# Kernel optimization log

Measured on AMD Instinct MI355X. Metric: run time of the kernel, lower is better.

The kernel has to match this reference:

```python
import jax, jax.numpy as jnp
import numpy as np

INPUT_DIM = 100
LATENT_DIM = 128
HIDDEN_DIM = 64
BATCH = 16384


def setup_inputs() -> dict:
    key = jax.random.key(0)
    ku, k1, kb1, k2, kb2 = jax.random.split(key, 5)
    u = jax.random.normal(ku, (BATCH, INPUT_DIM), dtype=jnp.float32)
    # PyTorch Linear init: U(-1/sqrt(fan_in), 1/sqrt(fan_in))
    s1 = 1.0 / np.sqrt(INPUT_DIM)
    s2 = 1.0 / np.sqrt(HIDDEN_DIM)
    W1 = jax.random.uniform(k1, (LATENT_DIM, HIDDEN_DIM, INPUT_DIM), jnp.float32, -s1, s1)
    b1 = jax.random.uniform(kb1, (LATENT_DIM, HIDDEN_DIM), jnp.float32, -s1, s1)
    W2 = jax.random.uniform(k2, (LATENT_DIM, HIDDEN_DIM), jnp.float32, -s2, s2)  # out_features=1 squeezed
    b2 = jax.random.uniform(kb2, (LATENT_DIM,), jnp.float32, -s2, s2)
    return {"u": u, "W1": W1, "b1": b1, "W2": W2, "b2": b2}


def reference(u, W1, b1, W2, b2):
    # All latent_dim branches batched as one grouped GEMM.
    # h: [batch, latent, hidden]
    h = jnp.tanh(jnp.einsum('bi,khi->bkh', u, W1) + b1[None, :, :])
    # out: [batch, latent]  (second Linear has output dim 1, squeezed)
    out = jnp.einsum('bkh,kh->bk', h, W2) + b2[None, :]
    return out
```

## Files before the change

### kernel.cpp

```cpp
#include <hip/hip_runtime.h>

#define BATCH 16384
#define LATENT 128
#define HIDDEN 64
#define INDIM 100
#define KPAD 128

typedef short shortx8 __attribute__((ext_vector_type(8)));
typedef float floatx4 __attribute__((ext_vector_type(4)));

__device__ __forceinline__ short f2bf(float f) {
    union { float f; unsigned u; } v; v.f = f;
    unsigned r = v.u + 0x7FFF + ((v.u >> 16) & 1);
    return (short)(r >> 16);
}

#if __has_builtin(__builtin_amdgcn_exp2f)
#define EXP2F(x) __builtin_amdgcn_exp2f(x)
#else
#define EXP2F(x) __exp2f(x)
#endif
#if __has_builtin(__builtin_amdgcn_rcpf)
#define RCPF(x) __builtin_amdgcn_rcpf(x)
#else
#define RCPF(x) (1.0f / (x))
#endif

#define DPP_REDUCE16(v) do {                                                              \
    v += __int_as_float(__builtin_amdgcn_update_dpp(0, __float_as_int(v), 0x128, 0xF, 0xF, true)); \
    v += __int_as_float(__builtin_amdgcn_update_dpp(0, __float_as_int(v), 0x124, 0xF, 0xF, true)); \
    v += __int_as_float(__builtin_amdgcn_update_dpp(0, __float_as_int(v), 0x122, 0xF, 0xF, true)); \
    v += __int_as_float(__builtin_amdgcn_update_dpp(0, __float_as_int(v), 0x121, 0xF, 0xF, true)); \
} while (0)

#define N_U_CHUNKS (BATCH * KPAD / 8)
#define N_W_CHUNKS (LATENT * HIDDEN * KPAD / 8)

__global__ __launch_bounds__(256) void prep_all(const float* __restrict__ u,
                                                const float* __restrict__ W1,
                                                const float* __restrict__ b1,
                                                shortx8* __restrict__ uf,
                                                shortx8* __restrict__ wf) {
    int c = blockIdx.x * 256 + threadIdx.x;
    if (c < N_U_CHUNKS) {
        int lane = c & 63;
        int kt = (c >> 6) & 3;
        int g = c >> 8;
        int row = g * 16 + (lane & 15);
        int kbase = kt * 32 + ((lane >> 4) << 3);
        shortx8 v;
        if (kbase + 7 < INDIM) {
            const float4* p = (const float4*)(u + row * INDIM + kbase);
            float4 f0 = p[0], f1 = p[1];
            v[0] = f2bf(f0.x); v[1] = f2bf(f0.y); v[2] = f2bf(f0.z); v[3] = f2bf(f0.w);
            v[4] = f2bf(f1.x); v[5] = f2bf(f1.y); v[6] = f2bf(f1.z); v[7] = f2bf(f1.w);
        } else {
#pragma unroll
            for (int j = 0; j < 8; j++) {
                int k = kbase + j;
                float f = (k < INDIM) ? u[row * INDIM + k] : (k == INDIM ? 1.0f : 0.0f);
                v[j] = f2bf(f);
            }
        }
        uf[c] = v;
    } else {
        int c2 = c - N_U_CHUNKS;
        int lane = c2 & 63;
        int kt = (c2 >> 6) & 3;
        int nt = (c2 >> 8) & 3;
        int lat = c2 >> 10;
        int h = nt * 16 + (lane & 15);
        int hw = lat * HIDDEN + h;
        int kbase = kt * 32 + ((lane >> 4) << 3);
        shortx8 v;
        if (kbase + 7 < INDIM) {
            const float4* p = (const float4*)(W1 + hw * INDIM + kbase);
            float4 f0 = p[0], f1 = p[1];
            v[0] = f2bf(f0.x); v[1] = f2bf(f0.y); v[2] = f2bf(f0.z); v[3] = f2bf(f0.w);
            v[4] = f2bf(f1.x); v[5] = f2bf(f1.y); v[6] = f2bf(f1.z); v[7] = f2bf(f1.w);
        } else {
#pragma unroll
            for (int j = 0; j < 8; j++) {
                int k = kbase + j;
                float f = (k < INDIM) ? W1[hw * INDIM + k] : (k == INDIM ? b1[hw] : 0.0f);
                v[j] = f2bf(f);
            }
        }
        wf[c2] = v;
    }
}

__global__ __launch_bounds__(256, 2) void branch_mlp(const shortx8* __restrict__ uf,
                                                     const shortx8* __restrict__ wf,
                                                     const float* __restrict__ W2,
                                                     const float* __restrict__ b2,
                                                     float* __restrict__ out) {
    int tid = threadIdx.x;
    int lane = tid & 63;
    int w = tid >> 6;
    int bx = blockIdx.x;
    int by = blockIdx.y;
    int g0 = bx * 8 + w * 2;
    int q = lane >> 4;
    int col = lane & 15;

    shortx8 a[2][4];
#pragma unroll
    for (int gi = 0; gi < 2; gi++)
#pragma unroll
        for (int kt = 0; kt < 4; kt++)
            a[gi][kt] = uf[((g0 + gi) * 4 + kt) * 64 + lane];

#pragma unroll
    for (int li = 0; li < 4; li++) {
        int lat = by * 4 + li;
        const shortx8* wfl = wf + (size_t)lat * 16 * 64;

        float w2v[4];
#pragma unroll
        for (int nt = 0; nt < 4; nt++) w2v[nt] = W2[lat * HIDDEN + nt * 16 + col];
        float b2v = b2[lat];

        floatx4 acc[2][4] = {};
#pragma unroll
        for (int kt = 0; kt < 4; kt++) {
#pragma unroll
            for (int nt = 0; nt < 4; nt++) {
                shortx8 bf = wfl[(nt * 4 + kt) * 64 + lane];
#pragma unroll
                for (int gi = 0; gi < 2; gi++)
                    acc[gi][nt] = __builtin_amdgcn_mfma_f32_16x16x32_bf16(a[gi][kt], bf, acc[gi][nt], 0, 0, 0);
            }
        }

#pragma unroll
        for (int gi = 0; gi < 2; gi++) {
            float p[4];
#pragma unroll
            for (int r = 0; r < 4; r++) {
                float s = 0.0f;
#pragma unroll
                for (int nt = 0; nt < 4; nt++) {
                    float x = acc[gi][nt][r];
                    float e = EXP2F(x * 2.88539008177793f);
                    float rr = RCPF(e + 1.0f);
                    float t = fmaf(-2.0f, rr, 1.0f);
                    s = fmaf(t, w2v[nt], s);
                }
                p[r] = s;
            }
#pragma unroll
            for (int r = 0; r < 4; r++) DPP_REDUCE16(p[r]);
            if (col == 0) {
                int rowbase = (g0 + gi) * 16 + q * 4;
#pragma unroll
                for (int r = 0; r < 4; r++)
                    out[(rowbase + r) * LATENT + lat] = p[r] + b2v;
            }
        }
    }
}

__global__ __launch_bounds__(256) void fallback_kernel(const float* __restrict__ u, const float* __restrict__ W1,
                                                       const float* __restrict__ b1, const float* __restrict__ W2,
                                                       const float* __restrict__ b2, float* __restrict__ out) {
    int idx = blockIdx.x * 256 + threadIdx.x;
    if (idx >= BATCH * LATENT) return;
    int b = idx >> 7;
    int lat = idx & 127;
    const float* ub = u + b * INDIM;
    float s = 0.0f;
    for (int h = 0; h < HIDDEN; h++) {
        const float* wp = W1 + (lat * HIDDEN + h) * INDIM;
        float d = b1[lat * HIDDEN + h];
        for (int k = 0; k < INDIM; k++) d += ub[k] * wp[k];
        s += tanhf(d) * W2[lat * HIDDEN + h];
    }
    out[idx] = s + b2[lat];
}

extern "C" void kernel_launch(void* const* d_in, const int* in_sizes, int n_in,
                              void* d_out, int out_size, void* d_ws, size_t ws_size,
                              hipStream_t stream) {
    const float* u  = (const float*)d_in[0];
    const float* W1 = (const float*)d_in[1];
    const float* b1 = (const float*)d_in[2];
    const float* W2 = (const float*)d_in[3];
    const float* b2 = (const float*)d_in[4];
    float* out = (float*)d_out;

    const size_t UF_BYTES = (size_t)BATCH * KPAD * 2;
    const size_t WF_BYTES = (size_t)LATENT * HIDDEN * KPAD * 2;

    if (ws_size < UF_BYTES + WF_BYTES) {
        fallback_kernel<<<(BATCH * LATENT + 255) / 256, 256, 0, stream>>>(u, W1, b1, W2, b2, out);
        return;
    }

    shortx8* uf = (shortx8*)d_ws;
    shortx8* wf = (shortx8*)((char*)d_ws + UF_BYTES);

    prep_all<<<(N_U_CHUNKS + N_W_CHUNKS) / 256, 256, 0, stream>>>(u, W1, b1, uf, wf);
    branch_mlp<<<dim3(BATCH / 128, LATENT / 4), 256, 0, stream>>>(uf, wf, W2, b2, out);
}
```

Baseline: 121.3 us.

## Swap MFMA operands so hidden lies along rows and reduce via cross-quad shuffles

Swaps the A/B operands of the MFMA so each lane's four accumulator registers hold consecutive hidden units for one batch row. The W2 dot product can then run mostly within each lane, using vector float4 loads of W2. The 16-lane DPP reduction over four partial sums becomes two xor shuffles over a single sum, and 16 lanes write 16 rows each. It also preloads all weight fragments before the MFMA loop and raises launch_bounds occupancy to 4 blocks, which risks register pressure and spills.

```diff
diff --git a/kernel.cpp b/kernel.cpp
--- a/kernel.cpp
+++ b/kernel.cpp
@@ -25,13 +25,6 @@
 #else
 #define RCPF(x) (1.0f / (x))
 #endif
-
-#define DPP_REDUCE16(v) do {                                                              \
-    v += __int_as_float(__builtin_amdgcn_update_dpp(0, __float_as_int(v), 0x128, 0xF, 0xF, true)); \
-    v += __int_as_float(__builtin_amdgcn_update_dpp(0, __float_as_int(v), 0x124, 0xF, 0xF, true)); \
-    v += __int_as_float(__builtin_amdgcn_update_dpp(0, __float_as_int(v), 0x122, 0xF, 0xF, true)); \
-    v += __int_as_float(__builtin_amdgcn_update_dpp(0, __float_as_int(v), 0x121, 0xF, 0xF, true)); \
-} while (0)
 
 #define N_U_CHUNKS (BATCH * KPAD / 8)
 #define N_W_CHUNKS (LATENT * HIDDEN * KPAD / 8)
@@ -90,7 +83,7 @@
     }
 }
 
-__global__ __launch_bounds__(256, 2) void branch_mlp(const shortx8* __restrict__ uf,
+__global__ __launch_bounds__(256, 4) void branch_mlp(const shortx8* __restrict__ uf,
                                                      const shortx8* __restrict__ wf,
                                                      const float* __restrict__ W2,
                                                      const float* __restrict__ b2,
@@ -102,61 +95,59 @@
     int by = blockIdx.y;
     int g0 = bx * 8 + w * 2;
     int q = lane >> 4;
-    int col = lane & 15;
 
-    shortx8 a[2][4];
+    shortx8 ub[2][4];
+    const shortx8* ua = uf + (size_t)g0 * 4 * 64 + lane;
 #pragma unroll
     for (int gi = 0; gi < 2; gi++)
 #pragma unroll
         for (int kt = 0; kt < 4; kt++)
-            a[gi][kt] = uf[((g0 + gi) * 4 + kt) * 64 + lane];
+            ub[gi][kt] = ua[(gi * 4 + kt) * 64];
 
 #pragma unroll
     for (int li = 0; li < 4; li++) {
         int lat = by * 4 + li;
-        const shortx8* wfl = wf + (size_t)lat * 16 * 64;
+        const shortx8* wb = wf + (size_t)lat * 16 * 64 + lane;
 
-        float w2v[4];
+        float4 w2v[4];
 #pragma unroll
-        for (int nt = 0; nt < 4; nt++) w2v[nt] = W2[lat * HIDDEN + nt * 16 + col];
+        for (int nt = 0; nt < 4; nt++)
+            w2v[nt] = *(const float4*)(W2 + lat * HIDDEN + nt * 16 + q * 4);
         float b2v = b2[lat];
+
+        shortx8 afr[4][4];
+#pragma unroll
+        for (int nt = 0; nt < 4; nt++)
+#pragma unroll
+            for (int kt = 0; kt < 4; kt++)
+                afr[nt][kt] = wb[(nt * 4 + kt) * 64];
 
         floatx4 acc[2][4] = {};
 #pragma unroll
-        for (int kt = 0; kt < 4; kt++) {
+        for (int kt = 0; kt < 4; kt++)
 #pragma unroll
-            for (int nt = 0; nt < 4; nt++) {
-                shortx8 bf = wfl[(nt * 4 + kt) * 64 + lane];
+            for (int nt = 0; nt < 4; nt++)
 #pragma unroll
                 for (int gi = 0; gi < 2; gi++)
-                    acc[gi][nt] = __builtin_amdgcn_mfma_f32_16x16x32_bf16(a[gi][kt], bf, acc[gi][nt], 0, 0, 0);
-            }
-        }
+                    acc[gi][nt] = __builtin_amdgcn_mfma_f32_16x16x32_bf16(afr[nt][kt], ub[gi][kt], acc[gi][nt], 0, 0, 0);
 
 #pragma unroll
         for (int gi = 0; gi < 2; gi++) {
-            float p[4];
+            float s = 0.0f;
 #pragma unroll
-            for (int r = 0; r < 4; r++) {
-                float s = 0.0f;
+            for (int nt = 0; nt < 4; nt++)
 #pragma unroll
-                for (int nt = 0; nt < 4; nt++) {
+                for (int r = 0; r < 4; r++) {
                     float x = acc[gi][nt][r];
                     float e = EXP2F(x * 2.88539008177793f);
                     float rr = RCPF(e + 1.0f);
                     float t = fmaf(-2.0f, rr, 1.0f);
-                    s = fmaf(t, w2v[nt], s);
+                    s = fmaf(t, w2v[nt][r], s);
                 }
-                p[r] = s;
-            }
-#pragma unroll
-            for (int r = 0; r < 4; r++) DPP_REDUCE16(p[r]);
-            if (col == 0) {
-                int rowbase = (g0 + gi) * 16 + q * 4;
-#pragma unroll
-                for (int r = 0; r < 4; r++)
-                    out[(rowbase + r) * LATENT + lat] = p[r] + b2v;
-            }
+            s += __shfl_xor(s, 16, 64);
+            s += __shfl_xor(s, 32, 64);
+            if (lane < 16)
+                out[((g0 + gi) * 16 + lane) * LATENT + lat] = s + b2v;
         }
     }
 }
@@ -172,9 +163,9 @@
     float s = 0.0f;
     for (int h = 0; h < HIDDEN; h++) {
         const float* wp = W1 + (lat * HIDDEN + h) * INDIM;
-        float d = b1[lat * HIDDEN + h];
-        for (int k = 0; k < INDIM; k++) d += ub[k] * wp[k];
-        s += tanhf(d) * W2[lat * HIDDEN + h];
+        float dd = b1[lat * HIDDEN + h];
+        for (int k = 0; k < INDIM; k++) dd += ub[k] * wp[k];
+        s += tanhf(dd) * W2[lat * HIDDEN + h];
     }
     out[idx] = s + b2[lat];
 }
```

New measurement: 124.7 us. 2.8% more time.
